# Performance work log

Measured on AMD Instinct MI355X. Metric: run time of the kernel, lower is better.

The kernel has to match this reference:

```python
import jax, jax.numpy as jnp
import numpy as np
from jax.scipy.special import gammaln

B, N, F, K = 128, 29, 64, 64
MAXZ, NITER, NPATH = 56, 2, 20
CUTOFF = 5.0


def setup_inputs() -> dict:
    key = jax.random.key(0)
    ks = jax.random.split(key, 16)
    atomic_numbers = jax.random.randint(ks[0], (B, N), 1, MAXZ)
    positions = jax.random.normal(ks[1], (B, N, 3), dtype=jnp.float32) * 2.0
    Ef = jax.random.normal(ks[2], (B, 3), dtype=jnp.float32)
    # fully connected molecular graph (all ordered pairs i != j), E = N*(N-1) = 812
    ii, jj = np.meshgrid(np.arange(N), np.arange(N), indexing="ij")
    m = ii != jj
    dst_idx = jnp.asarray(ii[m], dtype=jnp.int32)
    src_idx = jnp.asarray(jj[m], dtype=jnp.int32)
    s = 1.0 / np.sqrt(F)
    t = 0.2  # tensor-product path weight scale (keeps activations bounded)
    return {
        "atomic_numbers": atomic_numbers, "positions": positions, "Ef": Ef,
        "dst_idx": dst_idx, "src_idx": src_idx,
        "embed": jax.random.normal(ks[3], (MAXZ, F), dtype=jnp.float32) * s,
        "mp_basis_w": jax.random.normal(ks[4], (NITER, K, F), dtype=jnp.float32) / np.sqrt(K),
        "mp_tp_w": jax.random.normal(ks[5], (NITER, NPATH, F), dtype=jnp.float32) * t,
        "d1_w": jax.random.normal(ks[6], (NITER, 2, 2, F, F), dtype=jnp.float32) * s,
        "d1_b": jnp.zeros((NITER, 2, F), dtype=jnp.float32),
        "d2_w": jax.random.normal(ks[7], (NITER, 2, 2, F, F), dtype=jnp.float32) * s,
        "d2_b": jnp.zeros((NITER, 2, F), dtype=jnp.float32),
        "tens_w": jax.random.normal(ks[8], (NITER, NPATH, F), dtype=jnp.float32) * t,
        "td_dense_w": jax.random.normal(ks[9], (NITER, 2, 2, F, F), dtype=jnp.float32) * s,
        "td_tp_w": jax.random.normal(ks[10], (NITER, NPATH, F), dtype=jnp.float32) * t,
        "out_w": jax.random.normal(ks[11], (F,), dtype=jnp.float32) * s,
        "element_bias": jax.random.normal(ks[12], (MAXZ,), dtype=jnp.float32) * 0.1,
    }


def _tp(a, b, w):
    """Channelwise Clebsch-Gordan tensor product for max_degree=1 with parity channels.
    a, b: (M, 2, 4, F) with axis1 = (regular, pseudo), axis2 = (l=0, l=1 x/y/z).
    w: (20, F) learned per-path weights (5 l-paths x 4 parity combos)."""
    M, Fd = a.shape[0], a.shape[-1]
    sr = jnp.zeros((M, Fd), a.dtype); sp = jnp.zeros((M, Fd), a.dtype)
    vr = jnp.zeros((M, 3, Fd), a.dtype); vp = jnp.zeros((M, 3, Fd), a.dtype)
    idx = 0
    for p1 in range(2):
        for p2 in range(2):
            s1 = a[:, p1, 0]; v1 = a[:, p1, 1:4]
            s2 = b[:, p2, 0]; v2 = b[:, p2, 1:4]
            pl0a = 1 - 2 * p1; pl0b = 1 - 2 * p2   # parity of l=0 slot
            pl1a = -(1 - 2 * p1); pl1b = -(1 - 2 * p2)  # parity of l=1 slot
            tt = w[idx] * s1 * s2
            if pl0a * pl0b == 1: sr = sr + tt
            else: sp = sp + tt
            tt = w[idx + 1] * s1[:, None, :] * v2
            if pl0a * pl1b == -1: vr = vr + tt
            else: vp = vp + tt
            tt = w[idx + 2] * v1 * s2[:, None, :]
            if pl1a * pl0b == -1: vr = vr + tt
            else: vp = vp + tt
            tt = w[idx + 3] * jnp.sum(v1 * v2, axis=1)
            if pl1a * pl1b == 1: sr = sr + tt
            else: sp = sp + tt
            tt = w[idx + 4] * jnp.cross(v1, v2, axis=1)
            if pl1a * pl1b == -1: vr = vr + tt
            else: vp = vp + tt
            idx += 5
    reg = jnp.concatenate([sr[:, None, :], vr], axis=1)
    pse = jnp.concatenate([sp[:, None, :], vp], axis=1)
    return jnp.stack([reg, pse], axis=1)  # (M, 2, 4, F)


def _dense(x, W, b=None):
    # per-(parity, degree) linear map over features; W: (2, 2, F, F), b: (2, F)
    s = jnp.einsum("npf,pfg->npg", x[:, :, 0, :], W[:, 0])
    v = jnp.einsum("npdf,pfg->npdg", x[:, :, 1:4, :], W[:, 1])
    if b is not None:
        s = s + b
    return jnp.concatenate([s[:, :, None, :], v], axis=2)


def _silu(x):
    # gated equivariant silu: silu on scalars, sigmoid(scalar) gate on vectors
    s = x[:, :, 0:1, :]
    g = jax.nn.sigmoid(s)
    return jnp.concatenate([s * g, x[:, :, 1:4, :] * g], axis=2)


def _radial(r):
    # reciprocal Bernstein radial basis with smooth cutoff
    k = jnp.arange(K, dtype=r.dtype)
    logc = gammaln(float(K)) - gammaln(k + 1.0) - gammaln(float(K) - k)
    u = 1.0 / (1.0 + r)
    logb = logc + k * jnp.log(u)[:, None] + (K - 1.0 - k) * jnp.log(jnp.maximum(1.0 - u, 1e-12))[:, None]
    x2 = (r / CUTOFF) ** 2
    fcut = jnp.where(x2 < 1.0, jnp.exp(1.0 - 1.0 / jnp.maximum(1.0 - x2, 1e-12)), 0.0)
    return jnp.exp(logb) * fcut[:, None]  # (E, K)


def reference(atomic_numbers, positions, Ef, dst_idx, src_idx, embed, mp_basis_w,
              mp_tp_w, d1_w, d1_b, d2_w, d2_b, tens_w, td_dense_w, td_tp_w,
              out_w, element_bias):
    Bsz, Nn = atomic_numbers.shape
    BN = Bsz * Nn
    Fd = embed.shape[-1]
    pos = positions.reshape(-1, 3)
    Z = atomic_numbers.reshape(-1)
    offsets = (jnp.arange(Bsz, dtype=dst_idx.dtype) * Nn)
    dstf = (dst_idx[None, :] + offsets[:, None]).reshape(-1)  # (B*E,)
    srcf = (src_idx[None, :] + offsets[:, None]).reshape(-1)
    disp = pos[srcf] - pos[dstf]                               # (B*E, 3)
    r = jnp.sqrt(jnp.sum(disp * disp, axis=-1) + 1e-12)
    unit = disp / r[:, None]
    sph = jnp.concatenate([jnp.ones_like(r)[:, None], unit], axis=-1)  # (B*E, 4)
    basis = sph[:, :, None] * _radial(r)[:, None, :]           # (B*E, 4, K)

    x = jnp.zeros((BN, 2, 4, Fd), dtype=positions.dtype)
    x = x.at[:, 0, 0, :].set(embed[Z])

    xEFv = jnp.concatenate([jnp.ones((Bsz, 1), positions.dtype), Ef], axis=-1)  # (B, 4)
    xEF = jnp.repeat(xEFv, Nn, axis=0)                          # (BN, 4)
    xEF = jnp.broadcast_to(xEF[:, None, :, None], (BN, 2, 4, Fd))

    for i in range(NITER):
        bproj = jnp.einsum("edk,kf->edf", basis, mp_basis_w[i])  # (B*E, 4, F)
        bfeat = jnp.stack([bproj, jnp.zeros_like(bproj)], axis=1)  # (B*E, 2, 4, F)
        msg = _tp(x[srcf], bfeat, mp_tp_w[i])
        if i == NITER - 1:  # last iteration: max_degree=0 messages
            msg = msg * jnp.array([1.0, 0.0, 0.0, 0.0], msg.dtype)[None, None, :, None]
        y = jax.ops.segment_sum(msg, dstf, num_segments=BN)
        x = x + y
        h = _dense(x, d1_w[i], d1_b[i])
        h = _silu(h)
        h = _dense(h, d2_w[i], d2_b[i])
        x = h + y
        x = x + _tp(x, xEF, tens_w[i])          # Tensor()(x, xEF)
        x = _tp(x, _dense(x, td_dense_w[i]), td_tp_w[i])  # TensorDense

    s = x[:, 0, 0, :]  # degree-0 regular channel
    atomic_energies = s @ out_w + element_bias[Z]
    energy = atomic_energies.reshape(Bsz, Nn).sum(axis=1)
    return energy
```

## Files before the change

### kernel.cpp

```cpp
#include <hip/hip_runtime.h>

#define NB 128
#define NA 29
#define BN (NB*NA)
#define FD 64
#define NBLK 464


__device__ __forceinline__ void tp20(const float* a, const float* bb,
                                     const float* w, float* o)
{
  #pragma unroll
  for (int p1 = 0; p1 < 2; ++p1) {
    #pragma unroll
    for (int p2 = 0; p2 < 2; ++p2) {
      const float* w5 = w + 5*(2*p1 + p2);
      const float s1 = a[p1*4+0], x1 = a[p1*4+1], y1 = a[p1*4+2], z1 = a[p1*4+3];
      const float s2 = bb[p2*4+0], x2 = bb[p2*4+1], y2 = bb[p2*4+2], z2 = bb[p2*4+3];
      const int so = (p1 == p2) ? 0 : 4;
      const int vo = 4 - so;
      o[so+0] += w5[0]*(s1*s2) + w5[3]*(x1*x2 + y1*y2 + z1*z2);
      o[so+1] += w5[1]*(s1*x2) + w5[2]*(x1*s2);
      o[so+2] += w5[1]*(s1*y2) + w5[2]*(y1*s2);
      o[so+3] += w5[1]*(s1*z2) + w5[2]*(z1*s2);
      o[vo+1] += w5[4]*(y1*z2 - z1*y2);
      o[vo+2] += w5[4]*(z1*x2 - x1*z2);
      o[vo+3] += w5[4]*(x1*y2 - y1*x2);
    }
  }
}

__device__ __forceinline__ void stage2(float* __restrict__ wst,
                                       const float* __restrict__ src, int tid)
{
  const float4* s = (const float4*)src;
  float4* d = (float4*)wst;
  #pragma unroll
  for (int i = 0; i < 8; ++i) d[tid + i*256] = s[tid + i*256];
}

__device__ __forceinline__ void denseP2(const float* __restrict__ wst,
                                        const float* __restrict__ rA,
                                        const float* __restrict__ rB,
                                        float bs, int g,
                                        float oA[4], float oB[4])
{
  float a0A = bs, a0B = bs;
  #pragma unroll
  for (int f4 = 0; f4 < 16; ++f4) {
    const float w0 = wst[(f4*4+0)*64+g], w1 = wst[(f4*4+1)*64+g];
    const float w2 = wst[(f4*4+2)*64+g], w3 = wst[(f4*4+3)*64+g];
    const float4 xA = *(const float4*)&rA[f4*4];
    const float4 xB = *(const float4*)&rB[f4*4];
    a0A += w0*xA.x + w1*xA.y + w2*xA.z + w3*xA.w;
    a0B += w0*xB.x + w1*xB.y + w2*xB.z + w3*xB.w;
  }
  oA[0] = a0A; oB[0] = a0B;
  float a1A = 0, a2A = 0, a3A = 0, a1B = 0, a2B = 0, a3B = 0;
  #pragma unroll
  for (int f4 = 0; f4 < 16; ++f4) {
    const float w0 = wst[4096+(f4*4+0)*64+g], w1 = wst[4096+(f4*4+1)*64+g];
    const float w2 = wst[4096+(f4*4+2)*64+g], w3 = wst[4096+(f4*4+3)*64+g];
    const float4 aA = *(const float4*)&rA[ 64+f4*4];
    const float4 bA = *(const float4*)&rA[128+f4*4];
    const float4 cA = *(const float4*)&rA[192+f4*4];
    const float4 aB = *(const float4*)&rB[ 64+f4*4];
    const float4 bB = *(const float4*)&rB[128+f4*4];
    const float4 cB = *(const float4*)&rB[192+f4*4];
    a1A += w0*aA.x + w1*aA.y + w2*aA.z + w3*aA.w;
    a2A += w0*bA.x + w1*bA.y + w2*bA.z + w3*bA.w;
    a3A += w0*cA.x + w1*cA.y + w2*cA.z + w3*cA.w;
    a1B += w0*aB.x + w1*aB.y + w2*aB.z + w3*aB.w;
    a2B += w0*bB.x + w1*bB.y + w2*bB.z + w3*bB.w;
    a3B += w0*cB.x + w1*cB.y + w2*cB.z + w3*cB.w;
  }
  oA[1] = a1A; oA[2] = a2A; oA[3] = a3A;
  oB[1] = a1B; oB[2] = a2B; oB[3] = a3B;
}

template<bool LAST>
__device__ __forceinline__ void fmsg_phase(
    float* __restrict__ ov, float (*y_sh)[4][FD],
    const int* __restrict__ Z, const float* __restrict__ pos,
    const float* __restrict__ src,
    const float* __restrict__ wtp, const float* __restrict__ Wb,
    float logc, int j, int tid, int lane, int wv)
{
  float* rads  = ov;
  float* emb   = ov + 1792;
  float* yred  = ov + 3648;
  float* elu   = ov + 4672;
  float* el1mu = ov + 4700;
  float* efc   = ov + 4728;
  float* us    = ov + 4756;
  const float kk = (float)lane;

  float wb[64];
  #pragma unroll
  for (int k = 0; k < 64; ++k) wb[k] = Wb[k*FD + lane];
  const float wm0 = wtp[0*FD + lane];
  const float wm1 = LAST ? 0.0f : wtp[1*FD + lane];
  const float wm3 = LAST ? wtp[3*FD + lane]  : 0.0f;
  const float wm5 = LAST ? wtp[10*FD + lane] : 0.0f;
  const float wm8 = LAST ? wtp[13*FD + lane] : 0.0f;

  for (int t = 0; t < 8; ++t) {
    const int bn = j + NBLK*t;
    const int b = bn / NA, n = bn - b*NA;
    __syncthreads();
    if (tid < 28) {
      const int jr = tid, jj = jr + (jr >= n ? 1 : 0);
      const float dx = pos[(b*NA+jj)*3+0] - pos[(b*NA+n)*3+0];
      const float dy = pos[(b*NA+jj)*3+1] - pos[(b*NA+n)*3+1];
      const float dz = pos[(b*NA+jj)*3+2] - pos[(b*NA+n)*3+2];
      const float r  = sqrtf(dx*dx + dy*dy + dz*dz + 1e-12f);
      const float ri = 1.0f / r;
      us[jr*3+0] = dx*ri; us[jr*3+1] = dy*ri; us[jr*3+2] = dz*ri;
      const float u = 1.0f/(1.0f + r);
      elu[jr]   = logf(u);
      el1mu[jr] = logf(fmaxf(1.0f - u, 1e-12f));
      const float x2 = (r*0.2f)*(r*0.2f);
      efc[jr] = (x2 < 1.0f) ? expf(1.0f - 1.0f/fmaxf(1.0f - x2, 1e-12f)) : 0.0f;
    }
    if constexpr (!LAST) {
      for (int idx = tid; idx < NA*FD; idx += 256)
        emb[idx] = src[Z[b*NA + (idx>>6)]*FD + (idx&63)];
    }
    __syncthreads();

    #pragma unroll
    for (int i = 0; i < 7; ++i) {
      const int e = wv*7 + i;
      rads[e*64 + lane] = expf(logc + kk*elu[e] + (63.0f - kk)*el1mu[e]) * efc[e];
    }
    float y0 = 0.0f, y1 = 0.0f, y2 = 0.0f, y3 = 0.0f, y4 = 0.0f;
    #pragma unroll
    for (int i = 0; i < 7; ++i) {
      const int jr = wv*7 + i;
      float a0 = 0.0f;
      #pragma unroll
      for (int k4 = 0; k4 < 16; ++k4) {
        const float4 rv = *(const float4*)&rads[jr*64 + k4*4];
        a0 += wb[k4*4+0]*rv.x + wb[k4*4+1]*rv.y + wb[k4*4+2]*rv.z + wb[k4*4+3]*rv.w;
      }
      const int jj = jr + (jr >= n ? 1 : 0);
      const float ux = us[jr*3+0], uy = us[jr*3+1], uz = us[jr*3+2];
      if constexpr (!LAST) {
        const float t0 = a0 * emb[jj*64 + lane];
        y0 += wm0*t0;
        const float t1 = wm1*t0;
        y1 += t1*ux; y2 += t1*uy; y3 += t1*uz;
      } else {
        const float* xj = src + (size_t)(b*NA + jj)*512 + lane;
        const float s1   = xj[0];
        const float dot1 = xj[64]*ux + xj[128]*uy + xj[192]*uz;
        const float s1p  = xj[256];
        const float dotp = xj[320]*ux + xj[384]*uy + xj[448]*uz;
        y0 += a0*(wm0*s1  + wm3*dot1);
        y4 += a0*(wm5*s1p + wm8*dotp);
      }
    }
    if constexpr (!LAST) {
      yred[(wv*4+0)*64+lane] = y0; yred[(wv*4+1)*64+lane] = y1;
      yred[(wv*4+2)*64+lane] = y2; yred[(wv*4+3)*64+lane] = y3;
    } else {
      yred[(wv*4+0)*64+lane] = y0; yred[(wv*4+1)*64+lane] = y4;
    }
    __syncthreads();
    if (wv == 0) {
      const int nch = LAST ? 2 : 4;
      for (int c = 0; c < nch; ++c) {
        y_sh[t][c][lane] = yred[(0*4+c)*64+lane] + yred[(1*4+c)*64+lane]
                         + yred[(2*4+c)*64+lane] + yred[(3*4+c)*64+lane];
      }
    }
  }
  __syncthreads();
}

template<bool LAST>
__device__ __forceinline__ void node_phase(
    float* __restrict__ ov, float (*y_sh)[4][FD],
    const float* __restrict__ c4_sh,
    const int* __restrict__ Z, const float* __restrict__ embed,
    const float* __restrict__ Ef,
    const float* __restrict__ d1w, const float* __restrict__ d1b,
    const float* __restrict__ d2w, const float* __restrict__ d2b,
    const float* __restrict__ tens_w, const float* __restrict__ tdw,
    const float* __restrict__ td_tp_w, const float* __restrict__ out_w,
    const float* __restrict__ ebias,
    float* __restrict__ xg, float* __restrict__ out, int j, int tid)
{
  float* wst  = ov;
  float* rows = ov + 8192;
  const int r = tid >> 6, g = tid & 63;
  const int iA = 2*r, iB = iA + 1;
  const int ndA = j + NBLK*iA, ndB = j + NBLK*iB;
  float* rowA = rows + iA*512;
  float* rowB = rows + iB*512;

  float yA[4], yB[4];
  float y0A = 0, y4A = 0, y0B = 0, y4B = 0;
  if constexpr (!LAST) {
    #pragma unroll
    for (int c = 0; c < 4; ++c) { yA[c] = y_sh[iA][c][g]; yB[c] = y_sh[iB][c][g]; }
    rowA[g] = embed[Z[ndA]*FD + g] + yA[0];
    rowB[g] = embed[Z[ndB]*FD + g] + yB[0];
    #pragma unroll
    for (int c = 1; c < 4; ++c) { rowA[c*64+g] = yA[c]; rowB[c*64+g] = yB[c]; }
  } else {
    y0A = y_sh[iA][0][g]; y4A = y_sh[iA][1][g];
    y0B = y_sh[iB][0][g]; y4B = y_sh[iB][1][g];
    #pragma unroll
    for (int pc = 0; pc < 8; ++pc) {
      float vA = xg[(size_t)ndA*512 + pc*64 + g];
      float vB = xg[(size_t)ndB*512 + pc*64 + g];
      if (pc == 0) { vA += y0A; vB += y0B; }
      if (pc == 4) { vA += y4A; vB += y4B; }
      rowA[pc*64+g] = vA; rowB[pc*64+g] = vB;
    }
  }
  stage2(wst, d1w, tid);
  __syncthreads();

  {
    float hA[4], hB[4];
    denseP2(wst, rowA, rowB, d1b[g], g, hA, hB);
    const float sA = 1.0f/(1.0f + expf(-hA[0]));
    const float sB = 1.0f/(1.0f + expf(-hB[0]));
    rowA[g] = hA[0]*sA; rowB[g] = hB[0]*sB;
    #pragma unroll
    for (int c = 1; c < 4; ++c) { rowA[c*64+g] = hA[c]*sA; rowB[c*64+g] = hB[c]*sB; }
  }
  __syncthreads();
  if constexpr (LAST) {
    stage2(wst, d1w + 8192, tid);
    __syncthreads();
    float hA[4], hB[4];
    denseP2(wst, rowA + 256, rowB + 256, d1b[64+g], g, hA, hB);
    const float sA = 1.0f/(1.0f + expf(-hA[0]));
    const float sB = 1.0f/(1.0f + expf(-hB[0]));
    rowA[256+g] = hA[0]*sA; rowB[256+g] = hB[0]*sB;
    #pragma unroll
    for (int c = 1; c < 4; ++c) { rowA[256+c*64+g] = hA[c]*sA; rowB[256+c*64+g] = hB[c]*sB; }
    __syncthreads();
  }
  stage2(wst, d2w, tid);
  __syncthreads();

  float x2A[8], x2B[8];
  {
    float oA[4], oB[4];
    denseP2(wst, rowA, rowB, d2b[g], g, oA, oB);
    #pragma unroll
    for (int c = 0; c < 4; ++c) { x2A[c] = oA[c]; x2B[c] = oB[c]; }
  }
  if constexpr (!LAST) {
    #pragma unroll
    for (int c = 0; c < 4; ++c) { x2A[c] += yA[c]; x2B[c] += yB[c]; }
    const float c4v = c4_sh[g];
    x2A[4] = c4v; x2B[4] = c4v;
    x2A[5] = x2A[6] = x2A[7] = 0.0f;
    x2B[5] = x2B[6] = x2B[7] = 0.0f;
  } else {
    x2A[0] += y0A; x2B[0] += y0B;
    __syncthreads();
    stage2(wst, d2w + 8192, tid);
    __syncthreads();
    float oA[4], oB[4];
    denseP2(wst, rowA + 256, rowB + 256, d2b[64+g], g, oA, oB);
    x2A[4] = oA[0] + y4A; x2A[5] = oA[1]; x2A[6] = oA[2]; x2A[7] = oA[3];
    x2B[4] = oB[0] + y4B; x2B[5] = oB[1]; x2B[6] = oB[2]; x2B[7] = oB[3];
  }

  float x3A[8], x3B[8];
  {
    float w20[20];
    #pragma unroll
    for (int q = 0; q < 20; ++q) w20[q] = tens_w[q*FD + g];
    const int bA = ndA / NA, bB = ndB / NA;
    {
      const float bbv[8] = {1.0f, Ef[bA*3+0], Ef[bA*3+1], Ef[bA*3+2],
                            1.0f, Ef[bA*3+0], Ef[bA*3+1], Ef[bA*3+2]};
      float o[8] = {0,0,0,0,0,0,0,0};
      tp20(x2A, bbv, w20, o);
      #pragma unroll
      for (int pc = 0; pc < 8; ++pc) { x3A[pc] = x2A[pc] + o[pc]; rowA[pc*64+g] = x3A[pc]; }
    }
    {
      const float bbv[8] = {1.0f, Ef[bB*3+0], Ef[bB*3+1], Ef[bB*3+2],
                            1.0f, Ef[bB*3+0], Ef[bB*3+1], Ef[bB*3+2]};
      float o[8] = {0,0,0,0,0,0,0,0};
      tp20(x2B, bbv, w20, o);
      #pragma unroll
      for (int pc = 0; pc < 8; ++pc) { x3B[pc] = x2B[pc] + o[pc]; rowB[pc*64+g] = x3B[pc]; }
    }
  }
  __syncthreads();
  stage2(wst, tdw, tid);
  __syncthreads();

  float tdA[8], tdB[8];
  {
    float oA[4], oB[4];
    denseP2(wst, rowA, rowB, 0.0f, g, oA, oB);
    #pragma unroll
    for (int c = 0; c < 4; ++c) { tdA[c] = oA[c]; tdB[c] = oB[c]; }
  }
  __syncthreads();
  stage2(wst, tdw + 8192, tid);
  __syncthreads();
  {
    float oA[4], oB[4];
    denseP2(wst, rowA + 256, rowB + 256, 0.0f, g, oA, oB);
    #pragma unroll
    for (int c = 0; c < 4; ++c) { tdA[4+c] = oA[c]; tdB[4+c] = oB[c]; }
  }

  if constexpr (LAST) {
    const float wa = td_tp_w[0*FD+g],  wb = td_tp_w[3*FD+g];
    const float wc = td_tp_w[15*FD+g], wd = td_tp_w[18*FD+g];
    const float ow = out_w[g];
    float pA = ow * (wa*(x3A[0]*tdA[0])
                   + wb*(x3A[1]*tdA[1] + x3A[2]*tdA[2] + x3A[3]*tdA[3])
                   + wc*(x3A[4]*tdA[4])
                   + wd*(x3A[5]*tdA[5] + x3A[6]*tdA[6] + x3A[7]*tdA[7]));
    float pB = ow * (wa*(x3B[0]*tdB[0])
                   + wb*(x3B[1]*tdB[1] + x3B[2]*tdB[2] + x3B[3]*tdB[3])
                   + wc*(x3B[4]*tdB[4])
                   + wd*(x3B[5]*tdB[5] + x3B[6]*tdB[6] + x3B[7]*tdB[7]));
    #pragma unroll
    for (int off = 32; off > 0; off >>= 1) {
      pA += __shfl_xor(pA, off, 64);
      pB += __shfl_xor(pB, off, 64);
    }
    if (g == 0) {
      atomicAdd(&out[ndA/NA], pA + ebias[Z[ndA]]);
      atomicAdd(&out[ndB/NA], pB + ebias[Z[ndB]]);
    }
  } else {
    float w20[20];
    #pragma unroll
    for (int q = 0; q < 20; ++q) w20[q] = td_tp_w[q*FD + g];
    {
      float o[8] = {0,0,0,0,0,0,0,0};
      tp20(x3A, tdA, w20, o);
      #pragma unroll
      for (int pc = 0; pc < 8; ++pc) xg[(size_t)ndA*512 + pc*64 + g] = o[pc];
    }
    {
      float o[8] = {0,0,0,0,0,0,0,0};
      tp20(x3B, tdB, w20, o);
      #pragma unroll
      for (int pc = 0; pc < 8; ++pc) xg[(size_t)ndB*512 + pc*64 + g] = o[pc];
    }
  }
}

template<bool LAST>
__global__ __launch_bounds__(256) void iter_kernel(
    const int*   __restrict__ Z,
    const float* __restrict__ pos,
    const float* __restrict__ Ef,
    const float* __restrict__ embed,
    const float* __restrict__ mpbw,
    const float* __restrict__ mptpw,
    const float* __restrict__ d1w, const float* __restrict__ d1b,
    const float* __restrict__ d2w, const float* __restrict__ d2b,
    const float* __restrict__ tensw,
    const float* __restrict__ tdw,
    const float* __restrict__ tdtpw,
    const float* __restrict__ outw,
    const float* __restrict__ ebias,
    float* __restrict__ xg,
    float* __restrict__ out)
{
  __shared__ float4 ovb[3072];
  __shared__ float y_sh[8][4][FD];
  __shared__ float c4_sh[FD];
  float* ov = (float*)ovb;

  const int j = blockIdx.x, tid = threadIdx.x, lane = tid & 63, wv = tid >> 6;
  const float kk = (float)lane;
  const float logc = lgammaf(64.0f) - lgammaf(kk + 1.0f) - lgammaf(64.0f - kk);

  if constexpr (!LAST) {
    if (j < NB && tid == 0) out[j] = 0.0f;
    float* sil = ov;
    if (tid < 64) { const float v = d1b[64+tid]; sil[tid] = v/(1.0f + expf(-v)); }
    __syncthreads();
    if (tid < 64) {
      float acc = d2b[64 + tid];
      for (int f = 0; f < 64; ++f) acc += d2w[8192 + f*64 + tid] * sil[f];
      c4_sh[tid] = acc;
    }
  }

  const float* src = LAST ? xg : embed;
  fmsg_phase<LAST>(ov, y_sh, Z, pos, src, mptpw, mpbw, logc, j, tid, lane, wv);
  node_phase<LAST>(ov, y_sh, c4_sh, Z, embed, Ef, d1w, d1b, d2w, d2b,
                   tensw, tdw, tdtpw, outw, ebias, xg, out, j, tid);
}

extern "C" void kernel_launch(void* const* d_in, const int* in_sizes, int n_in,
                              void* d_out, int out_size, void* d_ws, size_t ws_size,
                              hipStream_t stream)
{
  (void)in_sizes; (void)n_in; (void)out_size; (void)ws_size;
  const int*   Z     = (const int*)  d_in[0];
  const float* pos   = (const float*)d_in[1];
  const float* Ef    = (const float*)d_in[2];
  const float* embed = (const float*)d_in[5];
  const float* mpbw  = (const float*)d_in[6];
  const float* mptpw = (const float*)d_in[7];
  const float* d1w   = (const float*)d_in[8];
  const float* d1b   = (const float*)d_in[9];
  const float* d2w   = (const float*)d_in[10];
  const float* d2b   = (const float*)d_in[11];
  const float* tensw = (const float*)d_in[12];
  const float* tdw   = (const float*)d_in[13];
  const float* tdtpw = (const float*)d_in[14];
  const float* outw  = (const float*)d_in[15];
  const float* ebias = (const float*)d_in[16];
  float* out = (float*)d_out;
  float* xg  = (float*)d_ws;

  iter_kernel<false><<<NBLK, 256, 0, stream>>>(Z, pos, Ef, embed,
      mpbw, mptpw, d1w, d1b, d2w, d2b, tensw, tdw, tdtpw, outw, ebias,
      xg, out);
  iter_kernel<true><<<NBLK, 256, 0, stream>>>(Z, pos, Ef, embed,
      mpbw + 4096, mptpw + 1280, d1w + 16384, d1b + 128, d2w + 16384,
      d2b + 128, tensw + 1280, tdw + 16384, tdtpw + 1280, outw, ebias,
      xg, out);
}
```

Before: 131.0 us.

## Double block size to 512 threads, processing two nodes concurrently per phase

Raises the block size from 256 to 512 threads. The message phase now processes two target nodes at once, one per half-block, each half with its own scratch regions. The node phase gives each wave a single node instead of two per thread. This halves the per-thread serial work and register pressure in the dense steps and raises occupancy with only 464 blocks, at the cost of more shared memory per block and wider barriers.

```diff
diff --git a/kernel.cpp b/kernel.cpp
--- a/kernel.cpp
+++ b/kernel.cpp
@@ -5,6 +5,7 @@
 #define BN (NB*NA)
 #define FD 64
 #define NBLK 464
+#define TPB 512
 
 
 __device__ __forceinline__ void tp20(const float* a, const float* bb,
@@ -36,46 +37,35 @@
   const float4* s = (const float4*)src;
   float4* d = (float4*)wst;
   #pragma unroll
-  for (int i = 0; i < 8; ++i) d[tid + i*256] = s[tid + i*256];
-}
-
-__device__ __forceinline__ void denseP2(const float* __restrict__ wst,
-                                        const float* __restrict__ rA,
-                                        const float* __restrict__ rB,
-                                        float bs, int g,
-                                        float oA[4], float oB[4])
-{
-  float a0A = bs, a0B = bs;
+  for (int i = 0; i < 4; ++i) d[tid + i*512] = s[tid + i*512];
+}
+
+__device__ __forceinline__ void denseP1(const float* __restrict__ wst,
+                                        const float* __restrict__ rw,
+                                        float bs, int g, float o[4])
+{
+  float a0 = bs;
   #pragma unroll
   for (int f4 = 0; f4 < 16; ++f4) {
     const float w0 = wst[(f4*4+0)*64+g], w1 = wst[(f4*4+1)*64+g];
     const float w2 = wst[(f4*4+2)*64+g], w3 = wst[(f4*4+3)*64+g];
-    const float4 xA = *(const float4*)&rA[f4*4];
-    const float4 xB = *(const float4*)&rB[f4*4];
-    a0A += w0*xA.x + w1*xA.y + w2*xA.z + w3*xA.w;
-    a0B += w0*xB.x + w1*xB.y + w2*xB.z + w3*xB.w;
-  }
-  oA[0] = a0A; oB[0] = a0B;
-  float a1A = 0, a2A = 0, a3A = 0, a1B = 0, a2B = 0, a3B = 0;
+    const float4 xv = *(const float4*)&rw[f4*4];
+    a0 += w0*xv.x + w1*xv.y + w2*xv.z + w3*xv.w;
+  }
+  o[0] = a0;
+  float a1 = 0, a2 = 0, a3 = 0;
   #pragma unroll
   for (int f4 = 0; f4 < 16; ++f4) {
     const float w0 = wst[4096+(f4*4+0)*64+g], w1 = wst[4096+(f4*4+1)*64+g];
     const float w2 = wst[4096+(f4*4+2)*64+g], w3 = wst[4096+(f4*4+3)*64+g];
-    const float4 aA = *(const float4*)&rA[ 64+f4*4];
-    const float4 bA = *(const float4*)&rA[128+f4*4];
-    const float4 cA = *(const float4*)&rA[192+f4*4];
-    const float4 aB = *(const float4*)&rB[ 64+f4*4];
-    const float4 bB = *(const float4*)&rB[128+f4*4];
-    const float4 cB = *(const float4*)&rB[192+f4*4];
-    a1A += w0*aA.x + w1*aA.y + w2*aA.z + w3*aA.w;
-    a2A += w0*bA.x + w1*bA.y + w2*bA.z + w3*bA.w;
-    a3A += w0*cA.x + w1*cA.y + w2*cA.z + w3*cA.w;
-    a1B += w0*aB.x + w1*aB.y + w2*aB.z + w3*aB.w;
-    a2B += w0*bB.x + w1*bB.y + w2*bB.z + w3*bB.w;
-    a3B += w0*cB.x + w1*cB.y + w2*cB.z + w3*cB.w;
-  }
-  oA[1] = a1A; oA[2] = a2A; oA[3] = a3A;
-  oB[1] = a1B; oB[2] = a2B; oB[3] = a3B;
+    const float4 xa = *(const float4*)&rw[ 64+f4*4];
+    const float4 xb = *(const float4*)&rw[128+f4*4];
+    const float4 xc = *(const float4*)&rw[192+f4*4];
+    a1 += w0*xa.x + w1*xa.y + w2*xa.z + w3*xa.w;
+    a2 += w0*xb.x + w1*xb.y + w2*xb.z + w3*xb.w;
+    a3 += w0*xc.x + w1*xc.y + w2*xc.z + w3*xc.w;
+  }
+  o[1] = a1; o[2] = a2; o[3] = a3;
 }
 
 template<bool LAST>
@@ -86,13 +76,13 @@
     const float* __restrict__ wtp, const float* __restrict__ Wb,
     float logc, int j, int tid, int lane, int wv)
 {
-  float* rads  = ov;
-  float* emb   = ov + 1792;
-  float* yred  = ov + 3648;
-  float* elu   = ov + 4672;
-  float* el1mu = ov + 4700;
-  float* efc   = ov + 4728;
-  float* us    = ov + 4756;
+  const int h  = wv >> 2;
+  const int wr = wv & 3;
+  float* rads  = ov + h*1792;
+  float* emb   = ov + 3584 + h*1856;
+  float* yred  = ov + 7296 + h*1024;
+  float* geom  = ov + 9344 + h*168;
+  float* elu = geom, *el1mu = geom + 28, *efc = geom + 56, *us = geom + 84;
   const float kk = (float)lane;
 
   float wb[64];
@@ -104,39 +94,44 @@
   const float wm5 = LAST ? wtp[10*FD + lane] : 0.0f;
   const float wm8 = LAST ? wtp[13*FD + lane] : 0.0f;
 
-  for (int t = 0; t < 8; ++t) {
+  for (int s = 0; s < 4; ++s) {
+    const int t  = 2*s + h;
     const int bn = j + NBLK*t;
     const int b = bn / NA, n = bn - b*NA;
     __syncthreads();
-    if (tid < 28) {
-      const int jr = tid, jj = jr + (jr >= n ? 1 : 0);
-      const float dx = pos[(b*NA+jj)*3+0] - pos[(b*NA+n)*3+0];
-      const float dy = pos[(b*NA+jj)*3+1] - pos[(b*NA+n)*3+1];
-      const float dz = pos[(b*NA+jj)*3+2] - pos[(b*NA+n)*3+2];
+    if (tid < 56) {
+      const int hh = tid / 28, jr = tid - hh*28;
+      const int bnn = j + NBLK*(2*s + hh);
+      const int bb = bnn / NA, nn = bnn - bb*NA;
+      const int jj = jr + (jr >= nn ? 1 : 0);
+      float* gg = ov + 9344 + hh*168;
+      const float dx = pos[(bb*NA+jj)*3+0] - pos[(bb*NA+nn)*3+0];
+      const float dy = pos[(bb*NA+jj)*3+1] - pos[(bb*NA+nn)*3+1];
+      const float dz = pos[(bb*NA+jj)*3+2] - pos[(bb*NA+nn)*3+2];
       const float r  = sqrtf(dx*dx + dy*dy + dz*dz + 1e-12f);
       const float ri = 1.0f / r;
-      us[jr*3+0] = dx*ri; us[jr*3+1] = dy*ri; us[jr*3+2] = dz*ri;
+      gg[84+jr*3+0] = dx*ri; gg[84+jr*3+1] = dy*ri; gg[84+jr*3+2] = dz*ri;
       const float u = 1.0f/(1.0f + r);
-      elu[jr]   = logf(u);
-      el1mu[jr] = logf(fmaxf(1.0f - u, 1e-12f));
+      gg[jr]      = logf(u);
+      gg[28+jr]   = logf(fmaxf(1.0f - u, 1e-12f));
       const float x2 = (r*0.2f)*(r*0.2f);
-      efc[jr] = (x2 < 1.0f) ? expf(1.0f - 1.0f/fmaxf(1.0f - x2, 1e-12f)) : 0.0f;
+      gg[56+jr] = (x2 < 1.0f) ? expf(1.0f - 1.0f/fmaxf(1.0f - x2, 1e-12f)) : 0.0f;
     }
     if constexpr (!LAST) {
-      for (int idx = tid; idx < NA*FD; idx += 256)
+      for (int idx = (tid & 255); idx < NA*FD; idx += 256)
         emb[idx] = src[Z[b*NA + (idx>>6)]*FD + (idx&63)];
     }
     __syncthreads();
 
     #pragma unroll
     for (int i = 0; i < 7; ++i) {
-      const int e = wv*7 + i;
+      const int e = wr*7 + i;
       rads[e*64 + lane] = expf(logc + kk*elu[e] + (63.0f - kk)*el1mu[e]) * efc[e];
     }
     float y0 = 0.0f, y1 = 0.0f, y2 = 0.0f, y3 = 0.0f, y4 = 0.0f;
     #pragma unroll
     for (int i = 0; i < 7; ++i) {
-      const int jr = wv*7 + i;
+      const int jr = wr*7 + i;
       float a0 = 0.0f;
       #pragma unroll
       for (int k4 = 0; k4 < 16; ++k4) {
@@ -161,13 +156,13 @@
       }
     }
     if constexpr (!LAST) {
-      yred[(wv*4+0)*64+lane] = y0; yred[(wv*4+1)*64+lane] = y1;
-      yred[(wv*4+2)*64+lane] = y2; yred[(wv*4+3)*64+lane] = y3;
+      yred[(wr*4+0)*64+lane] = y0; yred[(wr*4+1)*64+lane] = y1;
+      yred[(wr*4+2)*64+lane] = y2; yred[(wr*4+3)*64+lane] = y3;
     } else {
-      yred[(wv*4+0)*64+lane] = y0; yred[(wv*4+1)*64+lane] = y4;
-    }
-    __syncthreads();
-    if (wv == 0) {
+      yred[(wr*4+0)*64+lane] = y0; yred[(wr*4+1)*64+lane] = y4;
+    }
+    __syncthreads();
+    if (wr == 0) {
       const int nch = LAST ? 2 : 4;
       for (int c = 0; c < nch; ++c) {
         y_sh[t][c][lane] = yred[(0*4+c)*64+lane] + yred[(1*4+c)*64+lane]
@@ -193,172 +188,133 @@
 {
   float* wst  = ov;
   float* rows = ov + 8192;
-  const int r = tid >> 6, g = tid & 63;
-  const int iA = 2*r, iB = iA + 1;
-  const int ndA = j + NBLK*iA, ndB = j + NBLK*iB;
-  float* rowA = rows + iA*512;
-  float* rowB = rows + iB*512;
-
-  float yA[4], yB[4];
-  float y0A = 0, y4A = 0, y0B = 0, y4B = 0;
+  const int wv = tid >> 6, g = tid & 63;
+  const int nd = j + NBLK*wv;
+  float* row = rows + wv*512;
+
+  float yv[4];
+  float y0 = 0, y4 = 0;
   if constexpr (!LAST) {
     #pragma unroll
-    for (int c = 0; c < 4; ++c) { yA[c] = y_sh[iA][c][g]; yB[c] = y_sh[iB][c][g]; }
-    rowA[g] = embed[Z[ndA]*FD + g] + yA[0];
-    rowB[g] = embed[Z[ndB]*FD + g] + yB[0];
-    #pragma unroll
-    for (int c = 1; c < 4; ++c) { rowA[c*64+g] = yA[c]; rowB[c*64+g] = yB[c]; }
+    for (int c = 0; c < 4; ++c) yv[c] = y_sh[wv][c][g];
+    row[g] = embed[Z[nd]*FD + g] + yv[0];
+    #pragma unroll
+    for (int c = 1; c < 4; ++c) row[c*64+g] = yv[c];
   } else {
-    y0A = y_sh[iA][0][g]; y4A = y_sh[iA][1][g];
-    y0B = y_sh[iB][0][g]; y4B = y_sh[iB][1][g];
+    y0 = y_sh[wv][0][g]; y4 = y_sh[wv][1][g];
     #pragma unroll
     for (int pc = 0; pc < 8; ++pc) {
-      float vA = xg[(size_t)ndA*512 + pc*64 + g];
-      float vB = xg[(size_t)ndB*512 + pc*64 + g];
-      if (pc == 0) { vA += y0A; vB += y0B; }
-      if (pc == 4) { vA += y4A; vB += y4B; }
-      rowA[pc*64+g] = vA; rowB[pc*64+g] = vB;
+      float v = xg[(size_t)nd*512 + pc*64 + g];
+      if (pc == 0) v += y0;
+      if (pc == 4) v += y4;
+      row[pc*64+g] = v;
     }
   }
   stage2(wst, d1w, tid);
   __syncthreads();
 
   {
-    float hA[4], hB[4];
-    denseP2(wst, rowA, rowB, d1b[g], g, hA, hB);
-    const float sA = 1.0f/(1.0f + expf(-hA[0]));
-    const float sB = 1.0f/(1.0f + expf(-hB[0]));
-    rowA[g] = hA[0]*sA; rowB[g] = hB[0]*sB;
-    #pragma unroll
-    for (int c = 1; c < 4; ++c) { rowA[c*64+g] = hA[c]*sA; rowB[c*64+g] = hB[c]*sB; }
+    float h0[4];
+    denseP1(wst, row, d1b[g], g, h0);
+    const float sg = 1.0f/(1.0f + expf(-h0[0]));
+    row[g] = h0[0]*sg;
+    #pragma unroll
+    for (int c = 1; c < 4; ++c) row[c*64+g] = h0[c]*sg;
   }
   __syncthreads();
   if constexpr (LAST) {
     stage2(wst, d1w + 8192, tid);
     __syncthreads();
-    float hA[4], hB[4];
-    denseP2(wst, rowA + 256, rowB + 256, d1b[64+g], g, hA, hB);
-    const float sA = 1.0f/(1.0f + expf(-hA[0]));
-    const float sB = 1.0f/(1.0f + expf(-hB[0]));
-    rowA[256+g] = hA[0]*sA; rowB[256+g] = hB[0]*sB;
-    #pragma unroll
-    for (int c = 1; c < 4; ++c) { rowA[256+c*64+g] = hA[c]*sA; rowB[256+c*64+g] = hB[c]*sB; }
+    float h1[4];
+    denseP1(wst, row + 256, d1b[64+g], g, h1);
+    const float sg = 1.0f/(1.0f + expf(-h1[0]));
+    row[256+g] = h1[0]*sg;
+    #pragma unroll
+    for (int c = 1; c < 4; ++c) row[256+c*64+g] = h1[c]*sg;
     __syncthreads();
   }
   stage2(wst, d2w, tid);
   __syncthreads();
 
-  float x2A[8], x2B[8];
-  {
-    float oA[4], oB[4];
-    denseP2(wst, rowA, rowB, d2b[g], g, oA, oB);
-    #pragma unroll
-    for (int c = 0; c < 4; ++c) { x2A[c] = oA[c]; x2B[c] = oB[c]; }
+  float x2[8];
+  {
+    float o0[4];
+    denseP1(wst, row, d2b[g], g, o0);
+    #pragma unroll
+    for (int c = 0; c < 4; ++c) x2[c] = o0[c];
   }
   if constexpr (!LAST) {
     #pragma unroll
-    for (int c = 0; c < 4; ++c) { x2A[c] += yA[c]; x2B[c] += yB[c]; }
-    const float c4v = c4_sh[g];
-    x2A[4] = c4v; x2B[4] = c4v;
-    x2A[5] = x2A[6] = x2A[7] = 0.0f;
-    x2B[5] = x2B[6] = x2B[7] = 0.0f;
+    for (int c = 0; c < 4; ++c) x2[c] += yv[c];
+    x2[4] = c4_sh[g];
+    x2[5] = x2[6] = x2[7] = 0.0f;
   } else {
-    x2A[0] += y0A; x2B[0] += y0B;
+    x2[0] += y0;
     __syncthreads();
     stage2(wst, d2w + 8192, tid);
     __syncthreads();
-    float oA[4], oB[4];
-    denseP2(wst, rowA + 256, rowB + 256, d2b[64+g], g, oA, oB);
-    x2A[4] = oA[0] + y4A; x2A[5] = oA[1]; x2A[6] = oA[2]; x2A[7] = oA[3];
-    x2B[4] = oB[0] + y4B; x2B[5] = oB[1]; x2B[6] = oB[2]; x2B[7] = oB[3];
-  }
-
-  float x3A[8], x3B[8];
+    float o1[4];
+    denseP1(wst, row + 256, d2b[64+g], g, o1);
+    x2[4] = o1[0] + y4; x2[5] = o1[1]; x2[6] = o1[2]; x2[7] = o1[3];
+  }
+
+  float x3[8];
   {
     float w20[20];
     #pragma unroll
     for (int q = 0; q < 20; ++q) w20[q] = tens_w[q*FD + g];
-    const int bA = ndA / NA, bB = ndB / NA;
-    {
-      const float bbv[8] = {1.0f, Ef[bA*3+0], Ef[bA*3+1], Ef[bA*3+2],
-                            1.0f, Ef[bA*3+0], Ef[bA*3+1], Ef[bA*3+2]};
-      float o[8] = {0,0,0,0,0,0,0,0};
-      tp20(x2A, bbv, w20, o);
-      #pragma unroll
-      for (int pc = 0; pc < 8; ++pc) { x3A[pc] = x2A[pc] + o[pc]; rowA[pc*64+g] = x3A[pc]; }
-    }
-    {
-      const float bbv[8] = {1.0f, Ef[bB*3+0], Ef[bB*3+1], Ef[bB*3+2],
-                            1.0f, Ef[bB*3+0], Ef[bB*3+1], Ef[bB*3+2]};
-      float o[8] = {0,0,0,0,0,0,0,0};
-      tp20(x2B, bbv, w20, o);
-      #pragma unroll
-      for (int pc = 0; pc < 8; ++pc) { x3B[pc] = x2B[pc] + o[pc]; rowB[pc*64+g] = x3B[pc]; }
-    }
+    const int b = nd / NA;
+    const float bbv[8] = {1.0f, Ef[b*3+0], Ef[b*3+1], Ef[b*3+2],
+                          1.0f, Ef[b*3+0], Ef[b*3+1], Ef[b*3+2]};
+    float o[8] = {0,0,0,0,0,0,0,0};
+    tp20(x2, bbv, w20, o);
+    #pragma unroll
+    for (int pc = 0; pc < 8; ++pc) { x3[pc] = x2[pc] + o[pc]; row[pc*64+g] = x3[pc]; }
   }
   __syncthreads();
   stage2(wst, tdw, tid);
   __syncthreads();
 
-  float tdA[8], tdB[8];
-  {
-    float oA[4], oB[4];
-    denseP2(wst, rowA, rowB, 0.0f, g, oA, oB);
-    #pragma unroll
-    for (int c = 0; c < 4; ++c) { tdA[c] = oA[c]; tdB[c] = oB[c]; }
+  float td[8];
+  {
+    float o0[4];
+    denseP1(wst, row, 0.0f, g, o0);
+    #pragma unroll
+    for (int c = 0; c < 4; ++c) td[c] = o0[c];
   }
   __syncthreads();
   stage2(wst, tdw + 8192, tid);
   __syncthreads();
   {
-    float oA[4], oB[4];
-    denseP2(wst, rowA + 256, rowB + 256, 0.0f, g, oA, oB);
-    #pragma unroll
-    for (int c = 0; c < 4; ++c) { tdA[4+c] = oA[c]; tdB[4+c] = oB[c]; }
+    float o1[4];
+    denseP1(wst, row + 256, 0.0f, g, o1);
+    #pragma unroll
+    for (int c = 0; c < 4; ++c) td[4+c] = o1[c];
   }
 
   if constexpr (LAST) {
     const float wa = td_tp_w[0*FD+g],  wb = td_tp_w[3*FD+g];
     const float wc = td_tp_w[15*FD+g], wd = td_tp_w[18*FD+g];
-    const float ow = out_w[g];
-    float pA = ow * (wa*(x3A[0]*tdA[0])
-                   + wb*(x3A[1]*tdA[1] + x3A[2]*tdA[2] + x3A[3]*tdA[3])
-                   + wc*(x3A[4]*tdA[4])
-                   + wd*(x3A[5]*tdA[5] + x3A[6]*tdA[6] + x3A[7]*tdA[7]));
-    float pB = ow * (wa*(x3B[0]*tdB[0])
-                   + wb*(x3B[1]*tdB[1] + x3B[2]*tdB[2] + x3B[3]*tdB[3])
-                   + wc*(x3B[4]*tdB[4])
-                   + wd*(x3B[5]*tdB[5] + x3B[6]*tdB[6] + x3B[7]*tdB[7]));
-    #pragma unroll
-    for (int off = 32; off > 0; off >>= 1) {
-      pA += __shfl_xor(pA, off, 64);
-      pB += __shfl_xor(pB, off, 64);
-    }
-    if (g == 0) {
-      atomicAdd(&out[ndA/NA], pA + ebias[Z[ndA]]);
-      atomicAdd(&out[ndB/NA], pB + ebias[Z[ndB]]);
-    }
+    float p = out_w[g] * (wa*(x3[0]*td[0])
+                        + wb*(x3[1]*td[1] + x3[2]*td[2] + x3[3]*td[3])
+                        + wc*(x3[4]*td[4])
+                        + wd*(x3[5]*td[5] + x3[6]*td[6] + x3[7]*td[7]));
+    #pragma unroll
+    for (int off = 32; off > 0; off >>= 1) p += __shfl_xor(p, off, 64);
+    if (g == 0) atomicAdd(&out[nd/NA], p + ebias[Z[nd]]);
   } else {
     float w20[20];
     #pragma unroll
     for (int q = 0; q < 20; ++q) w20[q] = td_tp_w[q*FD + g];
-    {
-      float o[8] = {0,0,0,0,0,0,0,0};
-      tp20(x3A, tdA, w20, o);
-      #pragma unroll
-      for (int pc = 0; pc < 8; ++pc) xg[(size_t)ndA*512 + pc*64 + g] = o[pc];
-    }
-    {
-      float o[8] = {0,0,0,0,0,0,0,0};
-      tp20(x3B, tdB, w20, o);
-      #pragma unroll
-      for (int pc = 0; pc < 8; ++pc) xg[(size_t)ndB*512 + pc*64 + g] = o[pc];
-    }
+    float o[8] = {0,0,0,0,0,0,0,0};
+    tp20(x3, td, w20, o);
+    #pragma unroll
+    for (int pc = 0; pc < 8; ++pc) xg[(size_t)nd*512 + pc*64 + g] = o[pc];
   }
 }
 
 template<bool LAST>
-__global__ __launch_bounds__(256) void iter_kernel(
+__global__ __launch_bounds__(TPB) void iter_kernel(
     const int*   __restrict__ Z,
     const float* __restrict__ pos,
     const float* __restrict__ Ef,
@@ -425,10 +381,10 @@
   float* out = (float*)d_out;
   float* xg  = (float*)d_ws;
 
-  iter_kernel<false><<<NBLK, 256, 0, stream>>>(Z, pos, Ef, embed,
+  iter_kernel<false><<<NBLK, TPB, 0, stream>>>(Z, pos, Ef, embed,
       mpbw, mptpw, d1w, d1b, d2w, d2b, tensw, tdw, tdtpw, outw, ebias,
       xg, out);
-  iter_kernel<true><<<NBLK, 256, 0, stream>>>(Z, pos, Ef, embed,
+  iter_kernel<true><<<NBLK, TPB, 0, stream>>>(Z, pos, Ef, embed,
       mpbw + 4096, mptpw + 1280, d1w + 16384, d1b + 128, d2w + 16384,
       d2b + 128, tensw + 1280, tdw + 16384, tdtpw + 1280, outw, ebias,
       xg, out);
```

Result: slower. 158.2 us (+20.7%).
